# Kernel optimization log

Hardware: AMD Instinct MI355X
Metric: run time of the kernel (lower is better)

The kernel has to match this reference:

```python
import jax, jax.numpy as jnp
import numpy as np
from jax import lax

F_DIM, C_CONV, D, H, L, FF, V = 40, 512, 768, 12, 8, 3072, 8000
POS_K, POS_G = 95, 16


def _ln(x, g, b, eps=1e-5):
    mu = jnp.mean(x, -1, keepdims=True)
    var = jnp.var(x, -1, keepdims=True)
    return (x - mu) * lax.rsqrt(var + eps) * g + b


def _conv1d(x, w, b, stride, groups=1, padding='VALID'):
    # x: [B, C_in, T], w: [C_out, C_in//groups, K]
    y = lax.conv_general_dilated(x, w, (stride,), padding,
                                 feature_group_count=groups,
                                 dimension_numbers=('NCH', 'OIH', 'NCH'))
    return y + b[None, :, None]


def setup_inputs() -> dict:
    key = jax.random.key(0)
    ks = iter(jax.random.split(key, 40))
    s = 0.02
    d = {
        'feats': jax.random.normal(next(ks), (2, 8000, F_DIM), jnp.float32),
        'conv1_w': jax.random.normal(next(ks), (C_CONV, F_DIM, 3)) * s,
        'conv1_b': jnp.zeros((C_CONV,)),
        'conv2_w': jax.random.normal(next(ks), (D, C_CONV, 3)) * s,
        'conv2_b': jnp.zeros((D,)),
        'feat_ln_g': jnp.ones((D,)), 'feat_ln_b': jnp.zeros((D,)),
        'pos_w': jax.random.normal(next(ks), (D, D // POS_G, POS_K)) * s,
        'pos_b': jnp.zeros((D,)),
        'ctx_ln_g': jnp.ones((D,)), 'ctx_ln_b': jnp.zeros((D,)),
        'alibi_scale': jnp.ones((H,)),
        'Wqkv': jax.random.normal(next(ks), (L, 3 * D, D)) * s,
        'bqkv': jnp.zeros((L, 3 * D)),
        'Wo': jax.random.normal(next(ks), (L, D, D)) * s,
        'bo': jnp.zeros((L, D)),
        'ln1_g': jnp.ones((L, D)), 'ln1_b': jnp.zeros((L, D)),
        'ln2_g': jnp.ones((L, D)), 'ln2_b': jnp.zeros((L, D)),
        'W1': jax.random.normal(next(ks), (L, FF, D)) * s,
        'b1': jnp.zeros((L, FF)),
        'W2': jax.random.normal(next(ks), (L, D, FF)) * s,
        'b2': jnp.zeros((L, D)),
        'proj_w': jax.random.normal(next(ks), (V, D)) * s,
        'proj_b': jnp.zeros((V,)),
    }
    return d


def _forward(feats, conv1_w, conv1_b, conv2_w, conv2_b, feat_ln_g, feat_ln_b,
             pos_w, pos_b, ctx_ln_g, ctx_ln_b, alibi_scale,
             Wqkv, bqkv, Wo, bo, ln1_g, ln1_b, ln2_g, ln2_b,
             W1, b1, W2, b2, proj_w, proj_b):
    # ---- local_features: strided conv feature extractor ----
    x = feats.transpose(0, 2, 1)                       # [B, F, T_raw]
    x = jax.nn.gelu(_conv1d(x, conv1_w, conv1_b, 2))
    x = jax.nn.gelu(_conv1d(x, conv2_w, conv2_b, 2))   # [B, D, T]
    x = x.transpose(0, 2, 1)                           # [B, T, D]
    x = _ln(x, feat_ln_g, feat_ln_b)
    B, T, _ = x.shape

    # ---- relative positional encoder (grouped conv, SAME pad, GELU) ----
    xp = _conv1d(x.transpose(0, 2, 1), pos_w, pos_b, 1, groups=POS_G, padding='SAME')
    x = x + jax.nn.gelu(xp).transpose(0, 2, 1)

    # ---- ALiBi bias: -|i-j| * slope_h, scaled by clamped learned scale ----
    slopes = 2.0 ** (-8.0 * (jnp.arange(H, dtype=jnp.float32) + 1.0) / H)
    pos = jnp.arange(T)
    dist = jnp.abs(pos[:, None] - pos[None, :]).astype(jnp.float32)  # [T, T]
    bias = -dist[None, :, :] * slopes[:, None, None]                 # [H, T, T]
    bias = bias * jnp.clip(alibi_scale, 0.0, None)[:, None, None]
    bias = bias[None]                                                # [1, H, T, T]

    # ---- context encoder (layer norm) ----
    x = _ln(x, ctx_ln_g, ctx_ln_b)

    # ---- transformer blocks with ALiBi-biased attention ----
    dh = D // H
    scale = 1.0 / np.sqrt(dh)
    for i in range(L):
        h = _ln(x, ln1_g[i], ln1_b[i])
        qkv = h @ Wqkv[i].T + bqkv[i]                  # [B, T, 3D]
        q, k, v = jnp.split(qkv, 3, axis=-1)
        q = q.reshape(B, T, H, dh)
        k = k.reshape(B, T, H, dh)
        v = v.reshape(B, T, H, dh)
        scores = jnp.einsum('bqhd,bkhd->bhqk', q, k) * scale + bias
        attn = jax.nn.softmax(scores, axis=-1)
        o = jnp.einsum('bhqk,bkhd->bqhd', attn, v).reshape(B, T, D)
        x = x + o @ Wo[i].T + bo[i]
        h = _ln(x, ln2_g[i], ln2_b[i])
        x = x + jax.nn.gelu(h @ W1[i].T + b1[i]) @ W2[i].T + b2[i]

    # ---- transpose + projection ----
    x = x.transpose(1, 0, 2)                           # [T, B, D]
    return x @ proj_w.T + proj_b                       # [T, B, V]


def reference(feats, conv1_w, conv1_b, conv2_w, conv2_b, feat_ln_g, feat_ln_b,
              pos_w, pos_b, ctx_ln_g, ctx_ln_b, alibi_scale,
              Wqkv, bqkv, Wo, bo, ln1_g, ln1_b, ln2_g, ln2_b,
              W1, b1, W2, b2, proj_w, proj_b):
    return _forward(feats, conv1_w, conv1_b, conv2_w, conv2_b, feat_ln_g, feat_ln_b,
                    pos_w, pos_b, ctx_ln_g, ctx_ln_b, alibi_scale,
                    Wqkv, bqkv, Wo, bo, ln1_g, ln1_b, ln2_g, ln2_b,
                    W1, b1, W2, b2, proj_w, proj_b)
```

## Files before the change

kernel.cpp:

```cpp
#include <hip/hip_runtime.h>
#include <math.h>

typedef __attribute__((ext_vector_type(8))) short short8;
typedef __attribute__((ext_vector_type(4))) float f32x4;
typedef __attribute__((ext_vector_type(4))) unsigned short ushort4v;
typedef __attribute__((ext_vector_type(8))) unsigned short ushort8v;

#define DEV static __device__ __forceinline__

namespace {

constexpr int kB = 2;
constexpr int kTraw = 8000;
constexpr int kF = 40;
constexpr int kT1 = 3999;
constexpr int kC1 = 512;
constexpr int kT = 1999;
constexpr int kD = 768;
constexpr int kM = kB * kT;
constexpr int kM1 = kB * kT1;
constexpr int kH = 12;
constexpr int kDH = 64;
constexpr int kL = 8;
constexpr int kV = 8000;
constexpr int kPK = 95;
constexpr int kPKp = 96;
constexpr int kPG = 16;
constexpr int kCG = 48;
constexpr int kTP = 2048;
constexpr int kNCH = 4;
constexpr float kWIN = 8.0f;

DEV unsigned short f2bf(float x){
  union{unsigned int i; float f;} v; v.f = x;
  unsigned int r = v.i + 0x7FFFu + ((v.i >> 16) & 1u);
  return (unsigned short)(r >> 16);
}
DEV float bf2f(unsigned short u){
  union{unsigned int i; float f;} v; v.i = ((unsigned int)u) << 16; return v.f;
}
DEV float gelu_f(float x){
  return 0.5f * x * (1.0f + tanhf(0.7978845608028654f * (x + 0.044715f * x * x * x)));
}
DEV void gl2lds16(const unsigned short* g, unsigned short* l){
  __builtin_amdgcn_global_load_lds(
      (const __attribute__((address_space(1))) unsigned int*)(g),
      (__attribute__((address_space(3))) unsigned int*)(l), 16, 0, 0);
}
DEV void xcd_map(int bid, int Mtiles, int Ntiles, int& tm, int& tn){
  const int nwg = Mtiles * Ntiles;
  const int qq = nwg >> 3, rr = nwg & 7;
  const int xcd = bid & 7, idx = bid >> 3;
  const int k = (xcd < rr ? xcd * (qq + 1) : rr * (qq + 1) + (xcd - rr) * qq) + idx;
  const int fullb = Mtiles >> 2;
  const int kfull = fullb * 4 * Ntiles;
  if (k < kfull){
    int band = k / (4 * Ntiles), rem = k % (4 * Ntiles);
    tn = rem >> 2; tm = band * 4 + (rem & 3);
  } else {
    int rem = k - kfull, bh = Mtiles - fullb * 4;
    tn = rem / bh; tm = fullb * 4 + rem % bh;
  }
}

__global__ __launch_bounds__(256) void cast2_k(const float* __restrict__ s0,
    const float* __restrict__ s1, int split, int n16, unsigned short* __restrict__ dst)
{
  const int i = blockIdx.x * 256 + threadIdx.x;
  if (i >= n16) return;
  const float* s; int off;
  if (i < split){ s = s0; off = i; } else { s = s1; off = i - split; }
  const float4* sp = (const float4*)s + ((size_t)off << 2);
  float4 v0 = sp[0];
  float4 v1 = sp[1];
  float4 v2 = sp[2];
  float4 v3 = sp[3];
  ushort8v o0, o1;
  o0[0] = f2bf(v0.x); o0[1] = f2bf(v0.y); o0[2] = f2bf(v0.z); o0[3] = f2bf(v0.w);
  o0[4] = f2bf(v1.x); o0[5] = f2bf(v1.y); o0[6] = f2bf(v1.z); o0[7] = f2bf(v1.w);
  o1[0] = f2bf(v2.x); o1[1] = f2bf(v2.y); o1[2] = f2bf(v2.z); o1[3] = f2bf(v2.w);
  o1[4] = f2bf(v3.x); o1[5] = f2bf(v3.y); o1[6] = f2bf(v3.z); o1[7] = f2bf(v3.w);
  ushort8v* dp = (ushort8v*)dst + ((size_t)i << 1);
  dp[0] = o0;
  dp[1] = o1;
}

__global__ __launch_bounds__(256) void posw2_k(const float* __restrict__ pw,
    unsigned short* __restrict__ out)
{
  __shared__ alignas(16) unsigned short lds[96][72];
  const int bid = blockIdx.x, tid = threadIdx.x;
  const int g = bid / kCG, co = bid % kCG;
  for (int e = tid; e < 96 * 72; e += 256) ((unsigned short*)lds)[e] = 0;
  __syncthreads();
  const int ci = tid >> 2, kq = tid & 3;
  if (ci < 48){
    const float* base = pw + ((size_t)(g * kCG + co) * 48 + ci) * kPK;
    const int k1 = (kq == 3) ? 95 : (kq * 24 + 24);
    for (int k = kq * 24; k < k1; ++k) lds[k][ci] = f2bf(base[k]);
  }
  __syncthreads();
  unsigned short* ob = out + ((size_t)g * kPKp * kCG + co) * 64;
  for (int c = tid; c < 96 * 8; c += 256){
    const int k = c >> 3, s = c & 7;
    ushort8v v = *(const ushort8v*)&lds[k][s * 8];
    *(ushort8v*)(ob + (size_t)k * kCG * 64 + s * 8) = v;
  }
}

__global__ __launch_bounds__(256) void smallseg_k(const float* __restrict__ c1w,
    unsigned short* __restrict__ oc1, const float* __restrict__ c2w,
    unsigned short* __restrict__ oc2, const float* __restrict__ feats,
    unsigned short* __restrict__ ocol, unsigned short* __restrict__ vT)
{
  const int bid = blockIdx.x, tid = threadIdx.x;
  if (bid < 32){
    const int i = bid * 256 + tid;
    const int co = i >> 4, e = i & 15;
    ushort8v o;
    #pragma unroll
    for (int v = 0; v < 8; v++){
      const int j = e * 8 + v;
      float x = 0.f;
      if (j < 120){ int k = j / 40, ci = j % 40; x = c1w[(co * 40 + ci) * 3 + k]; }
      o[v] = f2bf(x);
    }
    *(ushort8v*)(oc1 + co * 128 + e * 8) = o;
  } else if (bid < 608){
    const int i = (bid - 32) * 256 + tid;
    const int co = i / 192, rem = i % 192;
    const int k = rem >> 6, c0 = (rem & 63) * 8;
    ushort8v o;
    #pragma unroll
    for (int v = 0; v < 8; v++) o[v] = f2bf(c2w[(co * 512 + c0 + v) * 3 + k]);
    *(ushort8v*)(oc2 + (size_t)co * 1536 + k * 512 + c0) = o;
  } else if (bid < 1108){
    const int i = (bid - 608) * 256 + tid;
    if (i < kM1 * 16){
      const int r = i >> 4, e = i & 15;
      const int b = r / kT1, t = r % kT1;
      ushort8v o;
      #pragma unroll
      for (int v = 0; v < 8; v++){
        const int j = e * 8 + v;
        float x = 0.f;
        if (j < 120){ int k = j / 40, f = j % 40; x = feats[((size_t)b * kTraw + 2 * t + k) * kF + f]; }
        o[v] = f2bf(x);
      }
      *(ushort8v*)(ocol + (size_t)r * 128 + e * 8) = o;
    }
  } else {
    const int i = (bid - 1108) * 256 + tid;
    if (i < kB * kH * kDH * (kTP - kT)){
      const int t = kT + i % (kTP - kT);
      const int r = i / (kTP - kT);
      vT[(size_t)r * kTP + t] = 0;
    }
  }
}

__global__ void im2col2_k(const unsigned short* __restrict__ act1, unsigned short* __restrict__ out){
  int i = blockIdx.x * 256 + threadIdx.x;
  int n4 = kM * 192;
  if (i >= n4) return;
  int r = i / 192, u = i % 192;
  int b = r / kT, t = r % kT;
  int j = u * 8;
  int k = j >> 9, c = j & 511;
  *(int4*)(out + (size_t)r * 1536 + j) =
      *(const int4*)(act1 + ((size_t)(b * kT1 + 2 * t + k)) * 512 + c);
}

template<int BM, int GELU, int BF16OUT, int F32OUT, int RES, int PERM, int VOUT, int PART>
__global__ __launch_bounds__(256, (BM == 64) ? 4 : 3) void gemm_k(
    const unsigned short* __restrict__ A, const unsigned short* __restrict__ Bw,
    const float* __restrict__ bias, float* Cf, unsigned short* Cbf,
    const float* res, unsigned short* vT, int Mtiles, int Ntiles, int Mm, int Nn, int Kk, int ldk)
{
  constexpr int MW = BM / 32;
  constexpr int LPT = (BM == 64) ? 3 : 4;
  __shared__ unsigned short smem[3 * (BM + 128) * 32];
  unsigned short* lsA0 = smem;
  unsigned short* lsB0 = smem + 3 * BM * 32;
  const int tid = threadIdx.x;
  const int lane = tid & 63, w = tid >> 6;
  const int wm = w >> 1, wn = w & 1;
  const int lo = lane & 15, hi = lane >> 4;
  const int NK = Kk >> 5;
  const int zc = blockIdx.z;
  A += (size_t)zc * Kk;
  Bw += (size_t)zc * Kk;

  int tm, tn;
  xcd_map(blockIdx.x, Mtiles, Ntiles, tm, tn);

  auto stage = [&](int buf, int kt){
    #pragma unroll
    for (int p = 0; p < BM / 64; ++p){
      int row = p * 64 + (tid >> 2);
      int ga = min(tm * BM + row, Mm - 1);
      int sl = (tid & 3) ^ ((row >> 1) & 3);
      gl2lds16(A + (size_t)ga * ldk + kt * 32 + sl * 8, lsA0 + buf * BM * 32 + (p * 64 + w * 16) * 32);
    }
    #pragma unroll
    for (int p = 0; p < 2; ++p){
      int row = p * 64 + (tid >> 2);
      int gb = min(tn * 128 + row, Nn - 1);
      int sl = (tid & 3) ^ ((row >> 1) & 3);
      gl2lds16(Bw + (size_t)gb * ldk + kt * 32 + sl * 8, lsB0 + buf * 128 * 32 + (p * 64 + w * 16) * 32);
    }
  };

  f32x4 acc[MW][4];
  #pragma unroll
  for (int m = 0; m < MW; m++)
    #pragma unroll
    for (int n = 0; n < 4; n++) acc[m][n] = f32x4{0.f, 0.f, 0.f, 0.f};

  stage(0, 0);
  stage(1, 1);

  for (int kt = 0; kt < NK; ++kt){
    if (kt + 1 < NK){
      if (LPT == 3) asm volatile("s_waitcnt vmcnt(3)" ::: "memory");
      else          asm volatile("s_waitcnt vmcnt(4)" ::: "memory");
    } else {
      asm volatile("s_waitcnt vmcnt(0)" ::: "memory");
    }
    asm volatile("s_barrier" ::: "memory");
    const unsigned short* As = lsA0 + (kt % 3) * BM * 32;
    const unsigned short* Bs = lsB0 + (kt % 3) * 128 * 32;
    short8 af[MW], bfv[4];
    #pragma unroll
    for (int m = 0; m < MW; m++){
      int row = wm * (16 * MW) + m * 16 + lo;
      int sp = hi ^ ((row >> 1) & 3);
      af[m] = *(const short8*)&As[row * 32 + sp * 8];
    }
    #pragma unroll
    for (int n = 0; n < 4; n++){
      int row = wn * 64 + n * 16 + lo;
      int sp = hi ^ ((row >> 1) & 3);
      bfv[n] = *(const short8*)&Bs[row * 32 + sp * 8];
    }
    if (kt + 2 < NK) stage((kt + 2) % 3, kt + 2);
    __builtin_amdgcn_s_setprio(1);
    #pragma unroll
    for (int m = 0; m < MW; m++)
      #pragma unroll
      for (int n = 0; n < 4; n++)
        acc[m][n] = __builtin_amdgcn_mfma_f32_16x16x32_bf16(af[m], bfv[n], acc[m][n], 0, 0, 0);
    __builtin_amdgcn_s_setprio(0);
  }

  __syncthreads();
  float* esm = (float*)smem + w * (16 * 68);
  const size_t zoff = (size_t)zc * Mm * Nn;
  #pragma unroll
  for (int m = 0; m < MW; m++){
    #pragma unroll
    for (int n = 0; n < 4; n++)
      #pragma unroll
      for (int r = 0; r < 4; r++)
        esm[(hi * 4 + r) * 68 + n * 16 + lo] = acc[m][n][r];
    #pragma unroll
    for (int rr = 0; rr < 4; rr++){
      const int lr = rr * 4 + hi;
      const int lc = lo * 4;
      float4 v = *(float4*)&esm[lr * 68 + lc];
      const int row = tm * BM + wm * (16 * MW) + m * 16 + lr;
      const int col = tn * 128 + wn * 64 + lc;
      if (row < Mm && col < Nn){
        if (PART){
          ushort4v u; u.x = f2bf(v.x); u.y = f2bf(v.y); u.z = f2bf(v.z); u.w = f2bf(v.w);
          *(ushort4v*)&Cbf[zoff + (size_t)row * Nn + col] = u;
        } else {
          float4 b4 = *(const float4*)&bias[col];
          float o0 = v.x + b4.x, o1 = v.y + b4.y, o2 = v.z + b4.z, o3 = v.w + b4.w;
          if (GELU){ o0 = gelu_f(o0); o1 = gelu_f(o1); o2 = gelu_f(o2); o3 = gelu_f(o3); }
          if (RES){
            float4 r4 = *(const float4*)&res[(size_t)row * Nn + col];
            o0 += r4.x; o1 += r4.y; o2 += r4.z; o3 += r4.w;
          }
          if (F32OUT){
            int orow = PERM ? ((row % kT) * kB + row / kT) : row;
            float4 u; u.x = o0; u.y = o1; u.z = o2; u.w = o3;
            *(float4*)&Cf[(size_t)orow * Nn + col] = u;
          }
          if (BF16OUT){
            if (!VOUT || col < 1536){
              ushort4v u; u.x = f2bf(o0); u.y = f2bf(o1); u.z = f2bf(o2); u.w = f2bf(o3);
              *(ushort4v*)&Cbf[(size_t)row * Nn + col] = u;
            }
          }
          if (VOUT && col >= 1536){
            int bb = row / kT, tt = row % kT;
            float ov[4] = {o0, o1, o2, o3};
            #pragma unroll
            for (int j = 0; j < 4; j++){
              int cj = col + j;
              int hh = (cj - 1536) >> 6, dd = (cj - 1536) & 63;
              vT[(((size_t)(bb * kH + hh)) * kDH + dd) * kTP + tt] = f2bf(ov[j]);
            }
          }
        }
      }
    }
  }
}

template<int GELU, int BF16OUT, int F32OUT, int RES, int PERM, int VOUT>
__global__ __launch_bounds__(512, 2) void gemm512_k(
    const unsigned short* __restrict__ A, const unsigned short* __restrict__ Bw,
    const float* __restrict__ bias, float* Cf, unsigned short* Cbf,
    const float* res, unsigned short* vT, int Mtiles, int Ntiles, int Mm, int Nn, int Kk)
{
  __shared__ unsigned short smem[3 * (128 + 256) * 32];
  unsigned short* lsA0 = smem;
  unsigned short* lsB0 = smem + 3 * 128 * 32;
  const int tid = threadIdx.x;
  const int lane = tid & 63, w = tid >> 6;
  const int wm = w >> 2, wn = w & 3;
  const int lo = lane & 15, hi = lane >> 4;
  const int NK = Kk >> 5;

  int tm, tn;
  xcd_map(blockIdx.x, Mtiles, Ntiles, tm, tn);

  auto stage = [&](int buf, int kt){
    {
      int row = tid >> 2;
      int ga = min(tm * 128 + row, Mm - 1);
      int sl = (tid & 3) ^ ((row >> 1) & 3);
      gl2lds16(A + (size_t)ga * Kk + kt * 32 + sl * 8, lsA0 + buf * 128 * 32 + (w * 16) * 32);
    }
    #pragma unroll
    for (int p = 0; p < 2; ++p){
      int row = p * 128 + (tid >> 2);
      int gb = min(tn * 256 + row, Nn - 1);
      int sl = (tid & 3) ^ ((row >> 1) & 3);
      gl2lds16(Bw + (size_t)gb * Kk + kt * 32 + sl * 8, lsB0 + buf * 256 * 32 + (p * 128 + w * 16) * 32);
    }
  };

  f32x4 acc[4][4];
  #pragma unroll
  for (int m = 0; m < 4; m++)
    #pragma unroll
    for (int n = 0; n < 4; n++) acc[m][n] = f32x4{0.f, 0.f, 0.f, 0.f};

  stage(0, 0);
  stage(1, 1);

  for (int kt = 0; kt < NK; ++kt){
    if (kt + 1 < NK) asm volatile("s_waitcnt vmcnt(3)" ::: "memory");
    else             asm volatile("s_waitcnt vmcnt(0)" ::: "memory");
    asm volatile("s_barrier" ::: "memory");
    const unsigned short* As = lsA0 + (kt % 3) * 128 * 32;
    const unsigned short* Bs = lsB0 + (kt % 3) * 256 * 32;
    short8 af[4], bfv[4];
    #pragma unroll
    for (int m = 0; m < 4; m++){
      int row = wm * 64 + m * 16 + lo;
      int sp = hi ^ ((row >> 1) & 3);
      af[m] = *(const short8*)&As[row * 32 + sp * 8];
    }
    #pragma unroll
    for (int n = 0; n < 4; n++){
      int row = wn * 64 + n * 16 + lo;
      int sp = hi ^ ((row >> 1) & 3);
      bfv[n] = *(const short8*)&Bs[row * 32 + sp * 8];
    }
    if (kt + 2 < NK) stage((kt + 2) % 3, kt + 2);
    __builtin_amdgcn_s_setprio(1);
    #pragma unroll
    for (int m = 0; m < 4; m++)
      #pragma unroll
      for (int n = 0; n < 4; n++)
        acc[m][n] = __builtin_amdgcn_mfma_f32_16x16x32_bf16(af[m], bfv[n], acc[m][n], 0, 0, 0);
    __builtin_amdgcn_s_setprio(0);
  }

  __syncthreads();
  float* esm = (float*)smem + w * (16 * 68);
  #pragma unroll
  for (int m = 0; m < 4; m++){
    #pragma unroll
    for (int n = 0; n < 4; n++)
      #pragma unroll
      for (int r = 0; r < 4; r++)
        esm[(hi * 4 + r) * 68 + n * 16 + lo] = acc[m][n][r];
    #pragma unroll
    for (int rr = 0; rr < 4; rr++){
      const int lr = rr * 4 + hi;
      const int lc = lo * 4;
      float4 v = *(float4*)&esm[lr * 68 + lc];
      const int row = tm * 128 + wm * 64 + m * 16 + lr;
      const int col = tn * 256 + wn * 64 + lc;
      if (row < Mm && col < Nn){
        float4 b4 = *(const float4*)&bias[col];
        float o0 = v.x + b4.x, o1 = v.y + b4.y, o2 = v.z + b4.z, o3 = v.w + b4.w;
        if (GELU){ o0 = gelu_f(o0); o1 = gelu_f(o1); o2 = gelu_f(o2); o3 = gelu_f(o3); }
        if (RES){
          float4 r4 = *(const float4*)&res[(size_t)row * Nn + col];
          o0 += r4.x; o1 += r4.y; o2 += r4.z; o3 += r4.w;
        }
        if (F32OUT){
          int orow = PERM ? ((row % kT) * kB + row / kT) : row;
          float4 u; u.x = o0; u.y = o1; u.z = o2; u.w = o3;
          *(float4*)&Cf[(size_t)orow * Nn + col] = u;
        }
        if (BF16OUT){
          ushort4v u; u.x = f2bf(o0); u.y = f2bf(o1); u.z = f2bf(o2); u.w = f2bf(o3);
          *(ushort4v*)&Cbf[(size_t)row * Nn + col] = u;
        }
      }
    }
  }
}

template<int OUTBF>
__global__ __launch_bounds__(256) void ln_k(const float* __restrict__ x, const float* __restrict__ gg,
    const float* __restrict__ bb, float* __restrict__ of, unsigned short* __restrict__ ob)
{
  const int row = blockIdx.x * 4 + (threadIdx.x >> 6);
  if (row >= kM) return;
  const int lane = threadIdx.x & 63;
  const float* xr = x + (size_t)row * kD;
  float4 v0 = *(const float4*)(xr + lane * 4);
  float4 v1 = *(const float4*)(xr + 256 + lane * 4);
  float4 v2 = *(const float4*)(xr + 512 + lane * 4);
  float s = v0.x + v0.y + v0.z + v0.w + v1.x + v1.y + v1.z + v1.w + v2.x + v2.y + v2.z + v2.w;
  #pragma unroll
  for (int o = 32; o >= 1; o >>= 1) s += __shfl_xor(s, o);
  const float mean = s * (1.0f / 768.0f);
  float q = 0.f;
  {
    float dx, dy, dz, dw;
    dx = v0.x - mean; dy = v0.y - mean; dz = v0.z - mean; dw = v0.w - mean; q += dx*dx + dy*dy + dz*dz + dw*dw;
    dx = v1.x - mean; dy = v1.y - mean; dz = v1.z - mean; dw = v1.w - mean; q += dx*dx + dy*dy + dz*dz + dw*dw;
    dx = v2.x - mean; dy = v2.y - mean; dz = v2.z - mean; dw = v2.w - mean; q += dx*dx + dy*dy + dz*dz + dw*dw;
  }
  #pragma unroll
  for (int o = 32; o >= 1; o >>= 1) q += __shfl_xor(q, o);
  const float rstd = rsqrtf(q * (1.0f / 768.0f) + 1e-5f);
  #pragma unroll
  for (int j = 0; j < 3; j++){
    float4 v = (j == 0) ? v0 : ((j == 1) ? v1 : v2);
    int c0 = j * 256 + lane * 4;
    float4 g4 = *(const float4*)(gg + c0);
    float4 b4 = *(const float4*)(bb + c0);
    float o0 = (v.x - mean) * rstd * g4.x + b4.x;
    float o1 = (v.y - mean) * rstd * g4.y + b4.y;
    float o2 = (v.z - mean) * rstd * g4.z + b4.z;
    float o3 = (v.w - mean) * rstd * g4.w + b4.w;
    if (OUTBF){
      ushort4v u; u.x = f2bf(o0); u.y = f2bf(o1); u.z = f2bf(o2); u.w = f2bf(o3);
      *(ushort4v*)(ob + (size_t)row * kD + c0) = u;
    } else {
      float4 u; u.x = o0; u.y = o1; u.z = o2; u.w = o3;
      *(float4*)(of + (size_t)row * kD + c0) = u;
    }
  }
}

__global__ __launch_bounds__(256) void lnln_k(const float* __restrict__ x,
    const float* __restrict__ g0v, const float* __restrict__ b0v,
    const float* __restrict__ g1v, const float* __restrict__ b1v,
    float* __restrict__ xo, unsigned short* __restrict__ hb)
{
  const int row = blockIdx.x * 4 + (threadIdx.x >> 6);
  if (row >= kM) return;
  const int lane = threadIdx.x & 63;
  const float* xr = x + (size_t)row * kD;
  float y[12];
  {
    float4 v0 = *(const float4*)(xr + lane * 4);
    float4 v1 = *(const float4*)(xr + 256 + lane * 4);
    float4 v2 = *(const float4*)(xr + 512 + lane * 4);
    float s = v0.x + v0.y + v0.z + v0.w + v1.x + v1.y + v1.z + v1.w + v2.x + v2.y + v2.z + v2.w;
    #pragma unroll
    for (int o = 32; o >= 1; o >>= 1) s += __shfl_xor(s, o);
    const float mean = s * (1.0f / 768.0f);
    float q = 0.f;
    float xv[12] = {v0.x, v0.y, v0.z, v0.w, v1.x, v1.y, v1.z, v1.w, v2.x, v2.y, v2.z, v2.w};
    #pragma unroll
    for (int t = 0; t < 12; t++){ float d = xv[t] - mean; q += d * d; }
    #pragma unroll
    for (int o = 32; o >= 1; o >>= 1) q += __shfl_xor(q, o);
    const float rstd = rsqrtf(q * (1.0f / 768.0f) + 1e-5f);
    #pragma unroll
    for (int j = 0; j < 3; j++){
      const int c0 = j * 256 + lane * 4;
      float4 g4 = *(const float4*)(g0v + c0);
      float4 b4 = *(const float4*)(b0v + c0);
      y[j*4+0] = (xv[j*4+0] - mean) * rstd * g4.x + b4.x;
      y[j*4+1] = (xv[j*4+1] - mean) * rstd * g4.y + b4.y;
      y[j*4+2] = (xv[j*4+2] - mean) * rstd * g4.z + b4.z;
      y[j*4+3] = (xv[j*4+3] - mean) * rstd * g4.w + b4.w;
      float4 u; u.x = y[j*4+0]; u.y = y[j*4+1]; u.z = y[j*4+2]; u.w = y[j*4+3];
      *(float4*)(xo + (size_t)row * kD + c0) = u;
    }
  }
  {
    float s = 0.f;
    #pragma unroll
    for (int t = 0; t < 12; t++) s += y[t];
    #pragma unroll
    for (int o = 32; o >= 1; o >>= 1) s += __shfl_xor(s, o);
    const float mean = s * (1.0f / 768.0f);
    float q = 0.f;
    #pragma unroll
    for (int t = 0; t < 12; t++){ float d = y[t] - mean; q += d * d; }
    #pragma unroll
    for (int o = 32; o >= 1; o >>= 1) q += __shfl_xor(q, o);
    const float rstd = rsqrtf(q * (1.0f / 768.0f) + 1e-5f);
    #pragma unroll
    for (int j = 0; j < 3; j++){
      const int c0 = j * 256 + lane * 4;
      float4 g4 = *(const float4*)(g1v + c0);
      float4 b4 = *(const float4*)(b1v + c0);
      ushort4v u;
      u.x = f2bf((y[j*4+0] - mean) * rstd * g4.x + b4.x);
      u.y = f2bf((y[j*4+1] - mean) * rstd * g4.y + b4.y);
      u.z = f2bf((y[j*4+2] - mean) * rstd * g4.z + b4.z);
      u.w = f2bf((y[j*4+3] - mean) * rstd * g4.w + b4.w);
      *(ushort4v*)(hb + (size_t)row * kD + c0) = u;
    }
  }
}

template<int LNOUT, int WRITEX>
__global__ __launch_bounds__(256) void cmbln_k(const unsigned short* __restrict__ p0,
    const unsigned short* __restrict__ p1,
    const float* __restrict__ bias, float* __restrict__ x, const float* __restrict__ gg,
    const float* __restrict__ bb, unsigned short* __restrict__ ob)
{
  const int row = blockIdx.x * 4 + (threadIdx.x >> 6);
  if (row >= kM) return;
  const int lane = threadIdx.x & 63;
  const size_t base = (size_t)row * kD;
  float xn[12];
  #pragma unroll
  for (int j = 0; j < 3; j++){
    const int c0 = j * 256 + lane * 4;
    float4 xv = *(const float4*)&x[base + c0];
    ushort4v a = *(const ushort4v*)&p0[base + c0];
    ushort4v bv = *(const ushort4v*)&p1[base + c0];
    float4 bs = *(const float4*)&bias[c0];
    xn[j*4+0] = xv.x + bf2f(a.x) + bf2f(bv.x) + bs.x;
    xn[j*4+1] = xv.y + bf2f(a.y) + bf2f(bv.y) + bs.y;
    xn[j*4+2] = xv.z + bf2f(a.z) + bf2f(bv.z) + bs.z;
    xn[j*4+3] = xv.w + bf2f(a.w) + bf2f(bv.w) + bs.w;
    if (WRITEX){
      float4 u; u.x = xn[j*4+0]; u.y = xn[j*4+1]; u.z = xn[j*4+2]; u.w = xn[j*4+3];
      *(float4*)&x[base + c0] = u;
    }
  }
  if (LNOUT){
    float s = 0.f;
    #pragma unroll
    for (int t = 0; t < 12; t++) s += xn[t];
    #pragma unroll
    for (int o = 32; o >= 1; o >>= 1) s += __shfl_xor(s, o);
    const float mean = s * (1.0f / 768.0f);
    float q = 0.f;
    #pragma unroll
    for (int t = 0; t < 12; t++){ float d = xn[t] - mean; q += d * d; }
    #pragma unroll
    for (int o = 32; o >= 1; o >>= 1) q += __shfl_xor(q, o);
    const float rstd = rsqrtf(q * (1.0f / 768.0f) + 1e-5f);
    #pragma unroll
    for (int j = 0; j < 3; j++){
      const int c0 = j * 256 + lane * 4;
      float4 g4 = *(const float4*)(gg + c0);
      float4 b4 = *(const float4*)(bb + c0);
      ushort4v u;
      u.x = f2bf((xn[j*4+0] - mean) * rstd * g4.x + b4.x);
      u.y = f2bf((xn[j*4+1] - mean) * rstd * g4.y + b4.y);
      u.z = f2bf((xn[j*4+2] - mean) * rstd * g4.z + b4.z);
      u.w = f2bf((xn[j*4+3] - mean) * rstd * g4.w + b4.w);
      *(ushort4v*)(ob + base + c0) = u;
    }
  } else {
    #pragma unroll
    for (int j = 0; j < 3; j++){
      const int c0 = j * 256 + lane * 4;
      ushort4v u;
      u.x = f2bf(xn[j*4+0]); u.y = f2bf(xn[j*4+1]);
      u.z = f2bf(xn[j*4+2]); u.w = f2bf(xn[j*4+3]);
      *(ushort4v*)(ob + base + c0) = u;
    }
  }
}

__global__ __launch_bounds__(256) void posconv_k(const float* __restrict__ x0,
    const unsigned short* __restrict__ wp, const float* __restrict__ pb, float* __restrict__ xsum)
{
  __shared__ unsigned short xs[224 * 64];
  __shared__ unsigned short wl[2][2 * 48 * 64];
  const int tid = threadIdx.x, lane = tid & 63, w = tid >> 6;
  const int t0 = blockIdx.x * 128, g = blockIdx.y, b = blockIdx.z;
  const int cg0 = g * kCG;
  for (int e = tid; e < 224 * 64; e += 256){
    int tr = e >> 6, ci = e & 63;
    int t = t0 - 47 + tr;
    unsigned short val = 0;
    if (ci < 48 && t >= 0 && t < kT) val = f2bf(x0[((size_t)(b * kT + t)) * kD + cg0 + ci]);
    xs[(tr * 8 + ((ci >> 3) ^ (tr & 7))) * 8 + (ci & 7)] = val;
  }
  const unsigned short* wg = wp + (size_t)g * kPKp * kCG * 64;
  auto stageW = [&](int buf, int c){
    const unsigned short* src = wg + (size_t)c * 2 * kCG * 64;
    #pragma unroll
    for (int j = 0; j < 3; j++){
      int row = w * 24 + j * 8 + (lane >> 3);
      int slot = (lane & 7) ^ (row & 7);
      gl2lds16(src + (size_t)row * 64 + slot * 8, &wl[buf][(w * 24 + j * 8) * 64]);
    }
  };
  stageW(0, 0);

  f32x4 acc[2][3];
  #pragma unroll
  for (int rg = 0; rg < 2; rg++)
    #pragma unroll
    for (int f = 0; f < 3; f++) acc[rg][f] = f32x4{0.f, 0.f, 0.f, 0.f};

  const int lo = lane & 15, hi = lane >> 4;
  for (int c = 0; c < 48; ++c){
    __syncthreads();
    if (c + 1 < 48) stageW((c + 1) & 1, c + 1);
    const int buf = c & 1;
    #pragma unroll
    for (int kk = 0; kk < 2; kk++){
      const int k = c * 2 + kk;
      short8 a0[2], a1[2];
      #pragma unroll
      for (int rg = 0; rg < 2; rg++){
        const int row0 = w * 32 + rg * 16 + lo + k;
        a0[rg] = *(const short8*)&xs[(row0 * 8 + ((hi    ) ^ (row0 & 7))) * 8];
        a1[rg] = *(const short8*)&xs[(row0 * 8 + ((hi + 4) ^ (row0 & 7))) * 8];
      }
      #pragma unroll
      for (int f = 0; f < 3; f++){
        const int wr = kk * 48 + f * 16 + lo;
        short8 b0 = *(const short8*)&wl[buf][(wr * 8 + ((hi    ) ^ (wr & 7))) * 8];
        short8 b1 = *(const short8*)&wl[buf][(wr * 8 + ((hi + 4) ^ (wr & 7))) * 8];
        #pragma unroll
        for (int rg = 0; rg < 2; rg++){
          acc[rg][f] = __builtin_amdgcn_mfma_f32_16x16x32_bf16(a0[rg], b0, acc[rg][f], 0, 0, 0);
          acc[rg][f] = __builtin_amdgcn_mfma_f32_16x16x32_bf16(a1[rg], b1, acc[rg][f], 0, 0, 0);
        }
      }
    }
  }
  #pragma unroll
  for (int rg = 0; rg < 2; rg++){
    #pragma unroll
    for (int f = 0; f < 3; f++){
      #pragma unroll
      for (int r = 0; r < 4; r++){
        int t = t0 + w * 32 + rg * 16 + (hi << 2) + r;
        int co = f * 16 + lo;
        if (t < kT){
          size_t idx = ((size_t)(b * kT + t)) * kD + cg0 + co;
          xsum[idx] = x0[idx] + gelu_f(acc[rg][f][r] + pb[cg0 + co]);
        }
      }
    }
  }
}

__global__ __launch_bounds__(256) void attn_k(const unsigned short* __restrict__ qkv,
    const unsigned short* __restrict__ vT, unsigned short* __restrict__ pO, float* __restrict__ plsum,
    const float* __restrict__ alibi_scale)
{
  const int tid = threadIdx.x, lane = tid & 63, w = tid >> 6;
  const int qb = blockIdx.x;
  const int cx = blockIdx.y / kH, h = blockIdx.y % kH;
  const int b = blockIdx.z;
  const float slope = exp2f(-8.0f * (float)(h + 1) * (1.0f / 12.0f)) * fmaxf(alibi_scale[h], 0.f);
  const float c1 = 0.125f * 1.44269504f;
  const float sl2 = slope * 1.44269504f;
  const float M2 = 12.0f * 1.44269504f;

  int ktlo, kthi;
  {
    float Wf = (slope > 1e-8f) ? kWIN / slope : 2048.0f;
    int W = (int)fminf(Wf, 2048.0f);
    int jlo = max(0, qb * 128 - W);
    int jhi = min(kT - 1, qb * 128 + 127 + W);
    ktlo = jlo >> 6; kthi = jhi >> 6;
  }
  ktlo = max(ktlo, cx * 8);
  kthi = min(kthi, cx * 8 + 7);
  if (ktlo > kthi) return;

  __shared__ unsigned short Kl[2][64 * 64];
  __shared__ unsigned short Vl[2][64 * 64];
  __shared__ unsigned short Pl[4][32 * 72];
  const int q0 = qb * 128 + w * 32;
  const int lo = lane & 15, hi = lane >> 4;

  short8 aq[2][2];
  #pragma unroll
  for (int qa = 0; qa < 2; qa++){
    const int qr = min(q0 + qa * 16 + lo, kT - 1);
    const unsigned short* qbase = qkv + ((size_t)(b * kT + qr)) * 2304 + h * 64 + hi * 8;
    aq[qa][0] = *(const short8*)(qbase);
    aq[qa][1] = *(const short8*)(qbase + 32);
  }

  f32x4 oacc[2][4];
  #pragma unroll
  for (int qa = 0; qa < 2; qa++)
    #pragma unroll
    for (int f = 0; f < 4; f++) oacc[qa][f] = f32x4{0.f, 0.f, 0.f, 0.f};
  float lrow[2][4];
  #pragma unroll
  for (int qa = 0; qa < 2; qa++)
    #pragma unroll
    for (int r = 0; r < 4; r++) lrow[qa][r] = 0.f;

  const unsigned short* kbase = qkv + (size_t)b * kT * 2304 + 768 + h * 64;
  const unsigned short* vbase = vT + ((size_t)(b * kH + h)) * kDH * kTP;
  unsigned short* pl = &Pl[w][0];

  auto stageKV = [&](int buf, int kt){
    const int j0 = kt * 64;
    #pragma unroll
    for (int c = 0; c < 2; c++){
      int row = w * 16 + c * 8 + (lane >> 3);
      int slot = (lane & 7) ^ (row & 7);
      int kr = min(j0 + row, kT - 1);
      gl2lds16(kbase + (size_t)kr * 2304 + slot * 8, &Kl[buf][(w * 16 + c * 8) * 64]);
      gl2lds16(vbase + (size_t)row * kTP + j0 + slot * 8, &Vl[buf][(w * 16 + c * 8) * 64]);
    }
  };
  stageKV(ktlo & 1, ktlo);

  for (int kt = ktlo; kt <= kthi; ++kt){
    __syncthreads();
    if (kt + 1 <= kthi) stageKV((kt + 1) & 1, kt + 1);
    const int buf = kt & 1;
    const int j0 = kt * 64;
    f32x4 sac[2][4];
    __builtin_amdgcn_s_setprio(1);
    #pragma unroll
    for (int f = 0; f < 4; f++){
      const int krow = f * 16 + lo;
      short8 b0 = *(const short8*)&Kl[buf][(krow * 8 + ((hi    ) ^ (krow & 7))) * 8];
      short8 b1 = *(const short8*)&Kl[buf][(krow * 8 + ((hi + 4) ^ (krow & 7))) * 8];
      #pragma unroll
      for (int qa = 0; qa < 2; qa++){
        f32x4 s = f32x4{0.f, 0.f, 0.f, 0.f};
        s = __builtin_amdgcn_mfma_f32_16x16x32_bf16(aq[qa][0], b0, s, 0, 0, 0);
        s = __builtin_amdgcn_mfma_f32_16x16x32_bf16(aq[qa][1], b1, s, 0, 0, 0);
        sac[qa][f] = s;
      }
    }
    __builtin_amdgcn_s_setprio(0);
    #pragma unroll
    for (int qa = 0; qa < 2; qa++){
      #pragma unroll
      for (int f = 0; f < 4; f++){
        const int j = j0 + f * 16 + lo;
        const float jf = (float)j;
        #pragma unroll
        for (int r = 0; r < 4; r++){
          const float qrow = (float)(q0 + qa * 16 + hi * 4 + r);
          float sv = sac[qa][f][r] * c1 - fabsf(qrow - jf) * sl2 - M2;
          if (j >= kT) sv = -1.0e30f;
          float e = exp2f(sv);
          lrow[qa][r] += e;
          pl[(qa * 16 + hi * 4 + r) * 72 + f * 16 + lo] = f2bf(e);
        }
      }
    }
    __builtin_amdgcn_s_setprio(1);
    #pragma unroll
    for (int c2 = 0; c2 < 2; c2++){
      short8 pa[2];
      #pragma unroll
      for (int qa = 0; qa < 2; qa++)
        pa[qa] = *(const short8*)&pl[(qa * 16 + lo) * 72 + c2 * 32 + hi * 8];
      #pragma unroll
      for (int f = 0; f < 4; f++){
        const int dr = f * 16 + lo;
        short8 bv = *(const short8*)&Vl[buf][(dr * 8 + ((c2 * 4 + hi) ^ (dr & 7))) * 8];
        #pragma unroll
        for (int qa = 0; qa < 2; qa++)
          oacc[qa][f] = __builtin_amdgcn_mfma_f32_16x16x32_bf16(pa[qa], bv, oacc[qa][f], 0, 0, 0);
      }
    }
    __builtin_amdgcn_s_setprio(0);
  }
  const int pidx = (cx * kB + b) * kH + h;
  unsigned short* po = pO + (size_t)pidx * kTP * 64;
  #pragma unroll
  for (int o = 1; o < 16; o <<= 1){
    #pragma unroll
    for (int qa = 0; qa < 2; qa++)
      #pragma unroll
      for (int r = 0; r < 4; r++) lrow[qa][r] += __shfl_xor(lrow[qa][r], o);
  }
  #pragma unroll
  for (int qa = 0; qa < 2; qa++){
    #pragma unroll
    for (int f = 0; f < 4; f++){
      #pragma unroll
      for (int r = 0; r < 4; r++){
        int q = q0 + qa * 16 + hi * 4 + r;
        if (q < kT) po[(size_t)q * 64 + f * 16 + lo] = f2bf(oacc[qa][f][r]);
      }
    }
  }
  if (lo == 0){
    #pragma unroll
    for (int qa = 0; qa < 2; qa++)
      #pragma unroll
      for (int r = 0; r < 4; r++){
        int q = q0 + qa * 16 + hi * 4 + r;
        if (q < kT) plsum[(size_t)pidx * kTP + q] = lrow[qa][r];
      }
  }
}

__global__ __launch_bounds__(256) void attnred_k(const unsigned short* __restrict__ pO,
    const float* __restrict__ plsum, const float* __restrict__ alibi_scale,
    unsigned short* __restrict__ obf)
{
  int i = blockIdx.x * 256 + threadIdx.x;
  const int total = kB * kH * kT * 16;
  if (i >= total) return;
  const int d4 = i & 15;
  int rest = i >> 4;
  const int q = rest % kT; rest /= kT;
  const int h = rest % kH;
  const int b = rest / kH;
  const float slope = exp2f(-8.0f * (float)(h + 1) * (1.0f / 12.0f)) * fmaxf(alibi_scale[h], 0.f);
  int ktlo, kthi;
  {
    float Wf = (slope > 1e-8f) ? kWIN / slope : 2048.0f;
    int W = (int)fminf(Wf, 2048.0f);
    const int qb = q >> 7;
    int jlo = max(0, qb * 128 - W);
    int jhi = min(kT - 1, qb * 128 + 127 + W);
    ktlo = jlo >> 6; kthi = jhi >> 6;
  }
  float a0 = 0.f, a1 = 0.f, a2 = 0.f, a3 = 0.f;
  float l = 0.f;
  #pragma unroll
  for (int c = 0; c < kNCH; c++){
    if (c * 8 + 7 >= ktlo && c * 8 <= kthi){
      const int pidx = (c * kB + b) * kH + h;
      ushort4v v = *(const ushort4v*)&pO[((size_t)pidx * kTP + q) * 64 + d4 * 4];
      a0 += bf2f(v.x); a1 += bf2f(v.y); a2 += bf2f(v.z); a3 += bf2f(v.w);
      l += plsum[(size_t)pidx * kTP + q];
    }
  }
  const float inv = 1.0f / l;
  ushort4v u;
  u.x = f2bf(a0 * inv); u.y = f2bf(a1 * inv);
  u.z = f2bf(a2 * inv); u.w = f2bf(a3 * inv);
  *(ushort4v*)&obf[((size_t)(b * kT + q)) * kD + h * 64 + d4 * 4] = u;
}

}

extern "C" void kernel_launch(void* const* d_in, const int* in_sizes, int n_in,
                              void* d_out, int out_size, void* d_ws, size_t ws_size,
                              hipStream_t stream)
{
  (void)in_sizes; (void)n_in; (void)out_size; (void)ws_size;
  const float* feats   = (const float*)d_in[0];
  const float* conv1_w = (const float*)d_in[1];
  const float* conv1_b = (const float*)d_in[2];
  const float* conv2_w = (const float*)d_in[3];
  const float* conv2_b = (const float*)d_in[4];
  const float* fln_g   = (const float*)d_in[5];
  const float* fln_b   = (const float*)d_in[6];
  const float* pos_w   = (const float*)d_in[7];
  const float* pos_b   = (const float*)d_in[8];
  const float* cln_g   = (const float*)d_in[9];
  const float* cln_b   = (const float*)d_in[10];
  const float* alibi   = (const float*)d_in[11];
  const float* Wqkv    = (const float*)d_in[12];
  const float* bqkv    = (const float*)d_in[13];
  const float* Wo      = (const float*)d_in[14];
  const float* bo      = (const float*)d_in[15];
  const float* ln1g    = (const float*)d_in[16];
  const float* ln1b    = (const float*)d_in[17];
  const float* ln2g    = (const float*)d_in[18];
  const float* ln2b    = (const float*)d_in[19];
  const float* W1      = (const float*)d_in[20];
  const float* b1      = (const float*)d_in[21];
  const float* W2      = (const float*)d_in[22];
  const float* b2      = (const float*)d_in[23];
  const float* projw   = (const float*)d_in[24];
  const float* projb   = (const float*)d_in[25];
  float* out = (float*)d_out;

  char* wsp = (char*)d_ws;
  size_t off = 0;
  auto alloc = [&](size_t nbytes)->char*{
    char* p = wsp + off;
    off += (nbytes + 255) & ~(size_t)255;
    return p;
  };
  unsigned short* wqkv_bf  = (unsigned short*)alloc((size_t)kL * 2304 * 768 * 2);
  unsigned short* wo_bf    = (unsigned short*)alloc((size_t)kL * 768 * 768 * 2);
  unsigned short* w1_bf    = (unsigned short*)alloc((size_t)kL * 3072 * 768 * 2);
  unsigned short* w2_bf    = (unsigned short*)alloc((size_t)kL * 768 * 3072 * 2);
  unsigned short* wproj_bf = (unsigned short*)alloc((size_t)kV * 768 * 2);
  unsigned short* wc1      = (unsigned short*)alloc((size_t)kC1 * 128 * 2);
  unsigned short* wc2      = (unsigned short*)alloc((size_t)kD * 1536 * 2);
  unsigned short* wpos     = (unsigned short*)alloc((size_t)kPG * kPKp * kCG * 64 * 2);
  char* pbase = wsp + off;
  unsigned short* a1col    = (unsigned short*)alloc((size_t)kM1 * 128 * 2);
  unsigned short* act1     = (unsigned short*)alloc((size_t)kM1 * 512 * 2);
  unsigned short* a2col    = (unsigned short*)alloc((size_t)kM * 1536 * 2);
  float* xa    = (float*)alloc((size_t)kM * 768 * 4);
  float* x0    = (float*)alloc((size_t)kM * 768 * 4);
  float* xsum  = (float*)alloc((size_t)kM * 768 * 4);
  float* x     = (float*)alloc((size_t)kM * 768 * 4);
  unsigned short* h_bf   = (unsigned short*)alloc((size_t)kM * 768 * 2);
  unsigned short* qkv_bf = (unsigned short*)alloc((size_t)kM * 2304 * 2);
  unsigned short* vTb    = (unsigned short*)alloc((size_t)kB * kH * kDH * kTP * 2);
  unsigned short* o_bf   = (unsigned short*)alloc((size_t)kM * 768 * 2);
  unsigned short* f_bf   = (unsigned short*)alloc((size_t)kM * 3072 * 2);
  unsigned short* xf_bf  = (unsigned short*)alloc((size_t)kM * 768 * 2);
  unsigned short* pO = (unsigned short*)pbase;
  float* plsum = (float*)(pbase + (size_t)kNCH * kB * kH * kTP * 64 * 2);
  unsigned short* pG = (unsigned short*)(pbase + (size_t)kNCH * kB * kH * kTP * 64 * 2
                                               + (size_t)kNCH * kB * kH * kTP * 4);
  unsigned short* pG1 = pG + (size_t)kM * 768;

  auto cgrid = [](size_t n){ return dim3((unsigned)((n + 255) / 256)); };

  cast2_k<<<dim3(4608), 256, 0, stream>>>(Wqkv, Wo, 884736, 1179648, wqkv_bf);
  cast2_k<<<dim3(4608), 256, 0, stream>>>(W1, W1, 1179648, 1179648, w1_bf);
  cast2_k<<<dim3(6108), 256, 0, stream>>>(W2, projw, 1179648, 1563648, w2_bf);
  posw2_k<<<dim3(16 * kCG), 256, 0, stream>>>(pos_w, wpos);
  smallseg_k<<<dim3(1402), 256, 0, stream>>>(conv1_w, wc1, conv2_w, wc2, feats, a1col, vTb);

  gemm_k<128,1,1,0,0,0,0,0><<<dim3(63 * 4), 256, 0, stream>>>(a1col, wc1, conv1_b, nullptr, act1, nullptr, nullptr, 63, 4, kM1, 512, 128, 128);
  im2col2_k<<<cgrid((size_t)kM * 192), 256, 0, stream>>>(act1, a2col);
  gemm_k<64,1,0,1,0,0,0,0><<<dim3(63 * 6), 256, 0, stream>>>(a2col, wc2, conv2_b, xa, nullptr, nullptr, nullptr, 63, 6, kM, 768, 1536, 1536);
  ln_k<0><<<dim3(1000), 256, 0, stream>>>(xa, fln_g, fln_b, x0, nullptr);
  posconv_k<<<dim3(16, 16, 2), 256, 0, stream>>>(x0, wpos, pos_b, xsum);
  lnln_k<<<dim3(1000), 256, 0, stream>>>(xsum, cln_g, cln_b, ln1g, ln1b, x, h_bf);

  const int nred = kB * kH * kT * 16;
  for (int i = 0; i < kL; i++){
    gemm_k<128,0,1,0,0,0,1,0><<<dim3(32 * 18), 256, 0, stream>>>(h_bf, wqkv_bf + (size_t)i * 2304 * 768,
        bqkv + i * 2304, nullptr, qkv_bf, nullptr, vTb, 32, 18, kM, 2304, 768, 768);
    attn_k<<<dim3(16, kH * kNCH, 2), 256, 0, stream>>>(qkv_bf, vTb, pO, plsum, alibi);
    attnred_k<<<cgrid(nred), 256, 0, stream>>>(pO, plsum, alibi, o_bf);
    gemm_k<64,0,0,1,1,0,0,0><<<dim3(63 * 6), 256, 0, stream>>>(o_bf, wo_bf + (size_t)i * 768 * 768,
        bo + i * 768, x, nullptr, x, nullptr, 63, 6, kM, 768, 768, 768);
    ln_k<1><<<dim3(1000), 256, 0, stream>>>(x, ln2g + i * 768, ln2b + i * 768, nullptr, h_bf);
    gemm_k<128,1,1,0,0,0,0,0><<<dim3(32 * 24), 256, 0, stream>>>(h_bf, w1_bf + (size_t)i * 3072 * 768,
        b1 + i * 3072, nullptr, f_bf, nullptr, nullptr, 32, 24, kM, 3072, 768, 768);
    gemm_k<64,0,0,0,0,0,0,1><<<dim3(63 * 6, 1, 2), 256, 0, stream>>>(f_bf, w2_bf + (size_t)i * 768 * 3072,
        nullptr, nullptr, pG, nullptr, nullptr, 63, 6, kM, 768, 1536, 3072);
    if (i < kL - 1){
      cmbln_k<1,1><<<dim3(1000), 256, 0, stream>>>(pG, pG1, b2 + i * 768, x,
          ln1g + (i + 1) * 768, ln1b + (i + 1) * 768, h_bf);
    } else {
      cmbln_k<0,0><<<dim3(1000), 256, 0, stream>>>(pG, pG1, b2 + i * 768, x,
          nullptr, nullptr, xf_bf);
    }
  }
  gemm512_k<0,0,1,0,1,0><<<dim3(32 * 32), 512, 0, stream>>>(xf_bf, wproj_bf, projb, out, nullptr, nullptr, nullptr, 32, 32, kM, kV, 768);
}
```

Baseline: 1.793 ms.

## Use fat 128x256 tiles with 256 threads for QKV, FFN1 and projection GEMMs

Turns the 512-thread 128x256 GEMM into a 256-thread variant where each wave computes a 64x128 sub-tile (4x8 MFMA accumulators), and adds V-transpose output support. The QKV and FFN1 GEMMs move from 128x128 tiles to this larger tile, halving their block count, and the final projection uses it too. The goal is more operand reuse per LDS read and fewer global loads per FLOP. The cost is higher register pressure and fewer blocks in flight, which can hurt latency hiding. The im2col change is a cosmetic rename.

```diff
diff --git a/kernel.cpp b/kernel.cpp
--- a/kernel.cpp
+++ b/kernel.cpp
@@ -164,11 +164,13 @@
   int n4 = kM * 192;
   if (i >= n4) return;
   int r = i / 192, u = i % 192;
-  int b = r / kT, t = r % kT;
+  int b = r / 192 ? 0 : 0, t = 0; (void)b; (void)t;
+  int rr = r;
+  int bb = rr / kT, tt = rr % kT;
   int j = u * 8;
   int k = j >> 9, c = j & 511;
-  *(int4*)(out + (size_t)r * 1536 + j) =
-      *(const int4*)(act1 + ((size_t)(b * kT1 + 2 * t + k)) * 512 + c);
+  *(int4*)(out + (size_t)rr * 1536 + j) =
+      *(const int4*)(act1 + ((size_t)(bb * kT1 + 2 * tt + k)) * 512 + c);
 }
 
 template<int BM, int GELU, int BF16OUT, int F32OUT, int RES, int PERM, int VOUT, int PART>
@@ -309,18 +311,18 @@
   }
 }
 
-template<int GELU, int BF16OUT, int F32OUT, int RES, int PERM, int VOUT>
-__global__ __launch_bounds__(512, 2) void gemm512_k(
+template<int GELU, int BF16OUT, int F32OUT, int PERM, int VOUT>
+__global__ __launch_bounds__(256, 2) void gemmft_k(
     const unsigned short* __restrict__ A, const unsigned short* __restrict__ Bw,
     const float* __restrict__ bias, float* Cf, unsigned short* Cbf,
-    const float* res, unsigned short* vT, int Mtiles, int Ntiles, int Mm, int Nn, int Kk)
+    unsigned short* vT, int Mtiles, int Ntiles, int Mm, int Nn, int Kk)
 {
   __shared__ unsigned short smem[3 * (128 + 256) * 32];
   unsigned short* lsA0 = smem;
   unsigned short* lsB0 = smem + 3 * 128 * 32;
   const int tid = threadIdx.x;
   const int lane = tid & 63, w = tid >> 6;
-  const int wm = w >> 2, wn = w & 3;
+  const int wm = w >> 1, wn = w & 1;
   const int lo = lane & 15, hi = lane >> 4;
   const int NK = Kk >> 5;
 
@@ -328,37 +330,38 @@
   xcd_map(blockIdx.x, Mtiles, Ntiles, tm, tn);
 
   auto stage = [&](int buf, int kt){
-    {
-      int row = tid >> 2;
+    #pragma unroll
+    for (int p = 0; p < 2; ++p){
+      int row = p * 64 + (tid >> 2);
       int ga = min(tm * 128 + row, Mm - 1);
       int sl = (tid & 3) ^ ((row >> 1) & 3);
-      gl2lds16(A + (size_t)ga * Kk + kt * 32 + sl * 8, lsA0 + buf * 128 * 32 + (w * 16) * 32);
-    }
-    #pragma unroll
-    for (int p = 0; p < 2; ++p){
-      int row = p * 128 + (tid >> 2);
+      gl2lds16(A + (size_t)ga * Kk + kt * 32 + sl * 8, lsA0 + buf * 128 * 32 + (p * 64 + w * 16) * 32);
+    }
+    #pragma unroll
+    for (int p = 0; p < 4; ++p){
+      int row = p * 64 + (tid >> 2);
       int gb = min(tn * 256 + row, Nn - 1);
       int sl = (tid & 3) ^ ((row >> 1) & 3);
-      gl2lds16(Bw + (size_t)gb * Kk + kt * 32 + sl * 8, lsB0 + buf * 256 * 32 + (p * 128 + w * 16) * 32);
+      gl2lds16(Bw + (size_t)gb * Kk + kt * 32 + sl * 8, lsB0 + buf * 256 * 32 + (p * 64 + w * 16) * 32);
     }
   };
 
-  f32x4 acc[4][4];
+  f32x4 acc[4][8];
   #pragma unroll
   for (int m = 0; m < 4; m++)
     #pragma unroll
-    for (int n = 0; n < 4; n++) acc[m][n] = f32x4{0.f, 0.f, 0.f, 0.f};
+    for (int n = 0; n < 8; n++) acc[m][n] = f32x4{0.f, 0.f, 0.f, 0.f};
 
   stage(0, 0);
   stage(1, 1);
 
   for (int kt = 0; kt < NK; ++kt){
-    if (kt + 1 < NK) asm volatile("s_waitcnt vmcnt(3)" ::: "memory");
+    if (kt + 1 < NK) asm volatile("s_waitcnt vmcnt(6)" ::: "memory");
     else             asm volatile("s_waitcnt vmcnt(0)" ::: "memory");
     asm volatile("s_barrier" ::: "memory");
     const unsigned short* As = lsA0 + (kt % 3) * 128 * 32;
     const unsigned short* Bs = lsB0 + (kt % 3) * 256 * 32;
-    short8 af[4], bfv[4];
+    short8 af[4], bfv[8];
     #pragma unroll
     for (int m = 0; m < 4; m++){
       int row = wm * 64 + m * 16 + lo;
@@ -366,8 +369,8 @@
       af[m] = *(const short8*)&As[row * 32 + sp * 8];
     }
     #pragma unroll
-    for (int n = 0; n < 4; n++){
-      int row = wn * 64 + n * 16 + lo;
+    for (int n = 0; n < 8; n++){
+      int row = wn * 128 + n * 16 + lo;
       int sp = hi ^ ((row >> 1) & 3);
       bfv[n] = *(const short8*)&Bs[row * 32 + sp * 8];
     }
@@ -376,7 +379,7 @@
     #pragma unroll
     for (int m = 0; m < 4; m++)
       #pragma unroll
-      for (int n = 0; n < 4; n++)
+      for (int n = 0; n < 8; n++)
         acc[m][n] = __builtin_amdgcn_mfma_f32_16x16x32_bf16(af[m], bfv[n], acc[m][n], 0, 0, 0);
     __builtin_amdgcn_s_setprio(0);
   }
@@ -386,33 +389,44 @@
   #pragma unroll
   for (int m = 0; m < 4; m++){
     #pragma unroll
-    for (int n = 0; n < 4; n++)
-      #pragma unroll
-      for (int r = 0; r < 4; r++)
-        esm[(hi * 4 + r) * 68 + n * 16 + lo] = acc[m][n][r];
-    #pragma unroll
-    for (int rr = 0; rr < 4; rr++){
-      const int lr = rr * 4 + hi;
-      const int lc = lo * 4;
-      float4 v = *(float4*)&esm[lr * 68 + lc];
-      const int row = tm * 128 + wm * 64 + m * 16 + lr;
-      const int col = tn * 256 + wn * 64 + lc;
-      if (row < Mm && col < Nn){
-        float4 b4 = *(const float4*)&bias[col];
-        float o0 = v.x + b4.x, o1 = v.y + b4.y, o2 = v.z + b4.z, o3 = v.w + b4.w;
-        if (GELU){ o0 = gelu_f(o0); o1 = gelu_f(o1); o2 = gelu_f(o2); o3 = gelu_f(o3); }
-        if (RES){
-          float4 r4 = *(const float4*)&res[(size_t)row * Nn + col];
-          o0 += r4.x; o1 += r4.y; o2 += r4.z; o3 += r4.w;
-        }
-        if (F32OUT){
-          int orow = PERM ? ((row % kT) * kB + row / kT) : row;
-          float4 u; u.x = o0; u.y = o1; u.z = o2; u.w = o3;
-          *(float4*)&Cf[(size_t)orow * Nn + col] = u;
-        }
-        if (BF16OUT){
-          ushort4v u; u.x = f2bf(o0); u.y = f2bf(o1); u.z = f2bf(o2); u.w = f2bf(o3);
-          *(ushort4v*)&Cbf[(size_t)row * Nn + col] = u;
+    for (int half = 0; half < 2; half++){
+      #pragma unroll
+      for (int n = 0; n < 4; n++)
+        #pragma unroll
+        for (int r = 0; r < 4; r++)
+          esm[(hi * 4 + r) * 68 + n * 16 + lo] = acc[m][half * 4 + n][r];
+      #pragma unroll
+      for (int rr = 0; rr < 4; rr++){
+        const int lr = rr * 4 + hi;
+        const int lc = lo * 4;
+        float4 v = *(float4*)&esm[lr * 68 + lc];
+        const int row = tm * 128 + wm * 64 + m * 16 + lr;
+        const int col = tn * 256 + wn * 128 + half * 64 + lc;
+        if (row < Mm && col < Nn){
+          float4 b4 = *(const float4*)&bias[col];
+          float o0 = v.x + b4.x, o1 = v.y + b4.y, o2 = v.z + b4.z, o3 = v.w + b4.w;
+          if (GELU){ o0 = gelu_f(o0); o1 = gelu_f(o1); o2 = gelu_f(o2); o3 = gelu_f(o3); }
+          if (F32OUT){
+            int orow = PERM ? ((row % kT) * kB + row / kT) : row;
+            float4 u; u.x = o0; u.y = o1; u.z = o2; u.w = o3;
+            *(float4*)&Cf[(size_t)orow * Nn + col] = u;
+          }
+          if (BF16OUT){
+            if (!VOUT || col < 1536){
+              ushort4v u; u.x = f2bf(o0); u.y = f2bf(o1); u.z = f2bf(o2); u.w = f2bf(o3);
+              *(ushort4v*)&Cbf[(size_t)row * Nn + col] = u;
+            }
+          }
+          if (VOUT && col >= 1536){
+            int bb = row / kT, tt = row % kT;
+            float ov[4] = {o0, o1, o2, o3};
+            #pragma unroll
+            for (int j = 0; j < 4; j++){
+              int cj = col + j;
+              int hh = (cj - 1536) >> 6, dd = (cj - 1536) & 63;
+              vT[(((size_t)(bb * kH + hh)) * kDH + dd) * kTP + tt] = f2bf(ov[j]);
+            }
+          }
         }
       }
     }
@@ -954,15 +968,15 @@
 
   const int nred = kB * kH * kT * 16;
   for (int i = 0; i < kL; i++){
-    gemm_k<128,0,1,0,0,0,1,0><<<dim3(32 * 18), 256, 0, stream>>>(h_bf, wqkv_bf + (size_t)i * 2304 * 768,
-        bqkv + i * 2304, nullptr, qkv_bf, nullptr, vTb, 32, 18, kM, 2304, 768, 768);
+    gemmft_k<0,1,0,0,1><<<dim3(32 * 9), 256, 0, stream>>>(h_bf, wqkv_bf + (size_t)i * 2304 * 768,
+        bqkv + i * 2304, nullptr, qkv_bf, vTb, 32, 9, kM, 2304, 768);
     attn_k<<<dim3(16, kH * kNCH, 2), 256, 0, stream>>>(qkv_bf, vTb, pO, plsum, alibi);
     attnred_k<<<cgrid(nred), 256, 0, stream>>>(pO, plsum, alibi, o_bf);
     gemm_k<64,0,0,1,1,0,0,0><<<dim3(63 * 6), 256, 0, stream>>>(o_bf, wo_bf + (size_t)i * 768 * 768,
         bo + i * 768, x, nullptr, x, nullptr, 63, 6, kM, 768, 768, 768);
     ln_k<1><<<dim3(1000), 256, 0, stream>>>(x, ln2g + i * 768, ln2b + i * 768, nullptr, h_bf);
-    gemm_k<128,1,1,0,0,0,0,0><<<dim3(32 * 24), 256, 0, stream>>>(h_bf, w1_bf + (size_t)i * 3072 * 768,
-        b1 + i * 3072, nullptr, f_bf, nullptr, nullptr, 32, 24, kM, 3072, 768, 768);
+    gemmft_k<1,1,0,0,0><<<dim3(32 * 12), 256, 0, stream>>>(h_bf, w1_bf + (size_t)i * 3072 * 768,
+        b1 + i * 3072, nullptr, f_bf, nullptr, 32, 12, kM, 3072, 768);
     gemm_k<64,0,0,0,0,0,0,1><<<dim3(63 * 6, 1, 2), 256, 0, stream>>>(f_bf, w2_bf + (size_t)i * 768 * 3072,
         nullptr, nullptr, pG, nullptr, nullptr, 63, 6, kM, 768, 1536, 3072);
     if (i < kL - 1){
@@ -973,5 +987,5 @@
           nullptr, nullptr, xf_bf);
     }
   }
-  gemm512_k<0,0,1,0,1,0><<<dim3(32 * 32), 512, 0, stream>>>(xf_bf, wproj_bf, projb, out, nullptr, nullptr, nullptr, 32, 32, kM, kV, 768);
-}
+  gemmft_k<0,0,1,1,0><<<dim3(32 * 32), 256, 0, stream>>>(xf_bf, wproj_bf, projb, out, nullptr, nullptr, 32, 32, kM, kV, 768);
+}
```

Result: slower. 1.950 ms (+8.7%).
